# Optimization experiments

Measured on AMD Instinct MI355X. Metric: run time of the kernel, lower is better.

## Reference

```python
import jax, jax.numpy as jnp
import numpy as np

B, S, IN, H = 16, 1024, 1024, 1024

def setup_inputs() -> dict:
    key = jax.random.key(0)
    k1, k2 = jax.random.split(key)
    x = jax.random.normal(k1, (B, S, IN), dtype=jnp.float32)
    # xavier_uniform with gain sqrt(2) over shape [2H, IN]
    limit = np.sqrt(2.0) * np.sqrt(6.0 / (2 * H + IN))
    W = jax.random.uniform(k2, (2 * H, IN), dtype=jnp.float32, minval=-limit, maxval=limit)
    return {"x": x, "W": W}

def reference(x, W):
    # i = x @ W.T -> [B, S, 2H]; split into key/value pre-activations
    i = jnp.einsum('bsi,oi->bso', x, W)
    ik, iv = jnp.split(i, 2, axis=2)          # each [B, S, H]
    mem0 = jnp.zeros((x.shape[0], H, H), dtype=x.dtype)

    def step(mem, kv):
        ik_t, iv_t = kv                        # [B, H] each
        k = jax.nn.relu(ik_t)
        v = jax.nn.relu(iv_t)
        # Hebbian plasticity rule: delta_mem = key outer val
        mem = mem + jnp.einsum('bk,bv->bkv', k, v)
        return mem, (k, v)

    # scan over time: move seq axis to front
    kv_seq = (jnp.swapaxes(ik, 0, 1), jnp.swapaxes(iv, 0, 1))  # [S, B, H]
    mem, (keys, vals) = jax.lax.scan(step, mem0, kv_seq)
    keys = jnp.swapaxes(keys, 0, 1)            # [B, S, H]
    vals = jnp.swapaxes(vals, 0, 1)
    return mem, keys, vals
```

## Files before the change

### kernel.cpp

```cpp
#include <hip/hip_runtime.h>

#define B_  16
#define S_  1024
#define IN_ 1024
#define H_  1024
#define N1  (2*H_)
#define M1  (B_*S_)
#define K1  IN_
#define XN  (M1*IN_)
#define WN  (N1*IN_)
#define LDG 1024

#define BM  256
#define BN  256
#define BK  64
#define CP  257

#define USZ  8192
#define ASZ  16384
#define TBUF 32768

typedef __attribute__((ext_vector_type(8))) short  short8;
typedef __attribute__((ext_vector_type(4))) float  floatx4;

__device__ __forceinline__ unsigned short f2bf(float f) {
    unsigned int u = __float_as_uint(f);
    u += 0x7fffu + ((u >> 16) & 1u);
    return (unsigned short)(u >> 16);
}

#define GLDS16(gp, lp) __builtin_amdgcn_global_load_lds(                      \
    (const __attribute__((address_space(1))) void*)(gp),                      \
    (__attribute__((address_space(3))) void*)(lp), 16, 0, 0)

#define WAITVM(N) { asm volatile("s_waitcnt vmcnt(" #N ")" ::: "memory");     \
                    __builtin_amdgcn_s_barrier();                             \
                    __builtin_amdgcn_sched_barrier(0); }

__global__ __launch_bounds__(256) void convert_kernel(
    const float* __restrict__ x, const float* __restrict__ W,
    unsigned short* __restrict__ xb, unsigned short* __restrict__ Wb)
{
    size_t i = ((size_t)blockIdx.x * 256 + threadIdx.x) * 8;
    const float* src;
    unsigned short* dst;
    if (i < (size_t)XN) { src = x + i; dst = xb + i; }
    else                { src = W + (i - XN); dst = Wb + (i - XN); }
    float4 a = *(const float4*)(src);
    float4 b = *(const float4*)(src + 4);
    ushort4 p = { f2bf(a.x), f2bf(a.y), f2bf(a.z), f2bf(a.w) };
    ushort4 q = { f2bf(b.x), f2bf(b.y), f2bf(b.z), f2bf(b.w) };
    *(ushort4*)(dst)     = p;
    *(ushort4*)(dst + 4) = q;
}

__device__ __forceinline__ void stage_u(
    const unsigned short* Ag, const unsigned short* Bg,
    unsigned short* buf, int op, int kh, int kt, int wave, int lane)
{
    const unsigned short* src = op ? Bg : Ag;
    unsigned short* dst = buf + op * ASZ + kh * USZ;
#pragma unroll
    for (int h = 0; h < 2; ++h) {
        int e   = (wave * 2 + h) * 64 + lane;
        int row = e >> 2, p = e & 3;
        int c   = p ^ (row & 3);
        GLDS16(src + (size_t)row * LDG + kt + kh * 32 + c * 8,
               dst + (wave * 2 + h) * 512);
    }
}

__device__ __forceinline__ void half_tile(
    const unsigned short* bufc, floatx4 (&acc)[8][4], int kc,
    const unsigned short* Ag, const unsigned short* Bg,
    unsigned short* bufn, int ktn, bool st,
    int wave, int lane, int wmw, int wnw, int quad, int r)
{
    const unsigned short* cA = bufc + kc * USZ;
    const unsigned short* cB = bufc + ASZ + kc * USZ;
    const int sw = (quad ^ (r & 3)) * 8;
    short8 bfr[4];
#pragma unroll
    for (int j = 0; j < 4; ++j)
        bfr[j] = *(const short8*)(cB + (wnw + j * 16 + r) * 32 + sw);
#pragma unroll
    for (int mh = 0; mh < 2; ++mh) {
        short8 af[4];
#pragma unroll
        for (int i = 0; i < 4; ++i)
            af[i] = *(const short8*)(cA + (wmw + (mh * 4 + i) * 16 + r) * 32 + sw);
        if (st) stage_u(Ag, Bg, bufn, mh, kc, ktn, wave, lane);
        __builtin_amdgcn_s_setprio(1);
#pragma unroll
        for (int i = 0; i < 4; ++i)
#pragma unroll
            for (int j = 0; j < 4; ++j)
                acc[mh * 4 + i][j] = __builtin_amdgcn_mfma_f32_16x16x32_bf16(
                    af[i], bfr[j], acc[mh * 4 + i][j], 0, 0, 0);
        __builtin_amdgcn_s_setprio(0);
    }
}

__device__ __forceinline__ void gemm_core(
    const unsigned short* Ag, const unsigned short* Bg,
    unsigned short* lds, floatx4 (&acc)[8][4], int wave, int lane)
{
    const int quad = lane >> 4, r = lane & 15;
    const int wmw  = (wave >> 2) * 128;
    const int wnw  = (wave & 3) * 64;

    stage_u(Ag, Bg, lds, 0, 0, 0, wave, lane);
    stage_u(Ag, Bg, lds, 1, 0, 0, wave, lane);
    stage_u(Ag, Bg, lds, 0, 1, 0, wave, lane);
    stage_u(Ag, Bg, lds, 1, 1, 0, wave, lane);

    for (int t = 0; t < 15; ++t) {
        unsigned short* bufc = lds + (t & 1) * TBUF;
        unsigned short* bufn = lds + ((t + 1) & 1) * TBUF;
        const int ktn = (t + 1) * BK;
        WAITVM(4)
        half_tile(bufc, acc, 0, Ag, Bg, bufn, ktn, true, wave, lane, wmw, wnw, quad, r);
        WAITVM(4)
        half_tile(bufc, acc, 1, Ag, Bg, bufn, ktn, true, wave, lane, wmw, wnw, quad, r);
    }
    {
        unsigned short* bufc = lds + TBUF;
        WAITVM(4)
        half_tile(bufc, acc, 0, Ag, Bg, bufc, 0, false, wave, lane, wmw, wnw, quad, r);
        WAITVM(0)
        half_tile(bufc, acc, 1, Ag, Bg, bufc, 0, false, wave, lane, wmw, wnw, quad, r);
    }
    __syncthreads();
}

__global__ __launch_bounds__(512, 2) void gemm1_kernel(
    const unsigned short* __restrict__ xb, const unsigned short* __restrict__ Wb,
    float* __restrict__ out,
    unsigned short* __restrict__ kT, unsigned short* __restrict__ vT)
{
    __shared__ unsigned short lds[65536];

    const int tid  = threadIdx.x;
    const int wave = tid >> 6, lane = tid & 63;
    const int quad = lane >> 4, r = lane & 15;
    const int wmw  = (wave >> 2) * 128;
    const int wnw  = (wave & 3) * 64;

    const int L   = blockIdx.x;
    const int xcd = L & 7, s = L >> 3;
    const int mt  = xcd * 8 + (s >> 3);
    const int nt  = s & 7;
    const int m0  = mt * BM, n0 = nt * BN;

    const unsigned short* Ag = xb + (size_t)m0 * K1;
    const unsigned short* Bg = Wb + (size_t)n0 * K1;

    floatx4 acc[8][4] = {};
    gemm_core(Ag, Bg, lds, acc, wave, lane);

    const bool isKeys = (nt < 4);
    float* outKV    = out + (isKeys ? (size_t)M1 * H_ : (size_t)2 * M1 * H_);
    const int ncol0 = isKeys ? n0 : (n0 - 1024);

#pragma unroll
    for (int f = 0; f < 8; ++f)
#pragma unroll
        for (int j = 0; j < 4; ++j)
#pragma unroll
            for (int d = 0; d < 4; ++d) {
                int row_l = wmw + f * 16 + quad * 4 + d;
                int col_l = wnw + j * 16 + r;
                outKV[(size_t)(m0 + row_l) * H_ + ncol0 + col_l] =
                    fmaxf(acc[f][j][d], 0.0f);
            }

    unsigned short* wsT = isKeys ? kT : vT;
    const int b  = m0 >> 10;
    const int s0 = m0 & 1023;
    unsigned short* dstB = wsT + (size_t)b * H_ * S_ + (size_t)ncol0 * S_ + s0;

#pragma unroll
    for (int ch = 0; ch < 2; ++ch) {
        if ((wave >> 2) == ch) {
#pragma unroll
            for (int f = 0; f < 8; ++f)
#pragma unroll
                for (int j = 0; j < 4; ++j)
#pragma unroll
                    for (int d = 0; d < 4; ++d) {
                        int lrow = f * 16 + quad * 4 + d;
                        int col  = wnw + j * 16 + r;
                        lds[lrow * CP + col] = f2bf(fmaxf(acc[f][j][d], 0.0f));
                    }
        }
        __syncthreads();
#pragma unroll
        for (int it = 0; it < 16; ++it) {
            int o   = it * 512 + tid;
            int n_l = o >> 5;
            int m4  = (o & 31) * 4;
            ushort4 v;
            v.x = lds[(m4 + 0) * CP + n_l];
            v.y = lds[(m4 + 1) * CP + n_l];
            v.z = lds[(m4 + 2) * CP + n_l];
            v.w = lds[(m4 + 3) * CP + n_l];
            *(ushort4*)(dstB + (size_t)n_l * S_ + ch * 128 + m4) = v;
        }
        __syncthreads();
    }
}

__global__ __launch_bounds__(512, 2) void gemm2_kernel(
    const unsigned short* __restrict__ kT, const unsigned short* __restrict__ vT,
    float* __restrict__ mem)
{
    __shared__ unsigned short lds[65536];

    const int tid  = threadIdx.x;
    const int wave = tid >> 6, lane = tid & 63;
    const int quad = lane >> 4, r = lane & 15;
    const int wmw  = (wave >> 2) * 128;
    const int wnw  = (wave & 3) * 64;

    const int L   = blockIdx.x;
    const int xcd = L & 7, s = L >> 3;
    const int b   = xcd * 2 + (s >> 4);
    const int tt  = s & 15;
    const int m0  = (tt >> 2) * BM;
    const int n0  = (tt & 3) * BN;

    const unsigned short* Ag = kT + (size_t)b * H_ * S_ + (size_t)m0 * S_;
    const unsigned short* Bg = vT + (size_t)b * H_ * S_ + (size_t)n0 * S_;

    floatx4 acc[8][4] = {};
    gemm_core(Ag, Bg, lds, acc, wave, lane);

    float* outb = mem + (size_t)b * H_ * H_;
#pragma unroll
    for (int f = 0; f < 8; ++f)
#pragma unroll
        for (int j = 0; j < 4; ++j)
#pragma unroll
            for (int d = 0; d < 4; ++d) {
                int row_l = wmw + f * 16 + quad * 4 + d;
                int col_l = wnw + j * 16 + r;
                outb[(size_t)(m0 + row_l) * H_ + n0 + col_l] = acc[f][j][d];
            }
}

extern "C" void kernel_launch(void* const* d_in, const int* in_sizes, int n_in,
                              void* d_out, int out_size, void* d_ws, size_t ws_size,
                              hipStream_t stream) {
    const float* x = (const float*)d_in[0];
    const float* W = (const float*)d_in[1];
    float* out = (float*)d_out;

    unsigned short* xb = (unsigned short*)d_out;
    unsigned short* Wb = xb + (size_t)XN;

    unsigned short* kT = (unsigned short*)d_ws;
    unsigned short* vT = kT + (size_t)B_ * H_ * S_;

    convert_kernel<<<dim3((XN + WN) / 2048), dim3(256), 0, stream>>>(x, W, xb, Wb);

    gemm1_kernel<<<dim3(512), dim3(512), 0, stream>>>(xb, Wb, out, kT, vT);

    gemm2_kernel<<<dim3(256), dim3(512), 0, stream>>>(kT, vT, out);
}
```

Before: 350.8 us.

## Fuse fp32-to-bf16 conversion of x into the GEMM1 A-tile load pipeline

Result: slower. 383.3 us (+9.3%).

```diff
diff --git a/kernel.cpp b/kernel.cpp
--- a/kernel.cpp
+++ b/kernel.cpp
@@ -7,9 +7,7 @@
 #define N1  (2*H_)
 #define M1  (B_*S_)
 #define K1  IN_
-#define XN  (M1*IN_)
 #define WN  (N1*IN_)
-#define LDG 1024
 
 #define BM  256
 #define BN  256
@@ -37,104 +35,93 @@
                     __builtin_amdgcn_s_barrier();                             \
                     __builtin_amdgcn_sched_barrier(0); }
 
-__global__ __launch_bounds__(256) void convert_kernel(
-    const float* __restrict__ x, const float* __restrict__ W,
-    unsigned short* __restrict__ xb, unsigned short* __restrict__ Wb)
+__global__ __launch_bounds__(256) void convert_w(
+    const float* __restrict__ W, unsigned short* __restrict__ Wb)
 {
     size_t i = ((size_t)blockIdx.x * 256 + threadIdx.x) * 8;
-    const float* src;
-    unsigned short* dst;
-    if (i < (size_t)XN) { src = x + i; dst = xb + i; }
-    else                { src = W + (i - XN); dst = Wb + (i - XN); }
-    float4 a = *(const float4*)(src);
-    float4 b = *(const float4*)(src + 4);
+    float4 a = *(const float4*)(W + i);
+    float4 b = *(const float4*)(W + i + 4);
     ushort4 p = { f2bf(a.x), f2bf(a.y), f2bf(a.z), f2bf(a.w) };
     ushort4 q = { f2bf(b.x), f2bf(b.y), f2bf(b.z), f2bf(b.w) };
-    *(ushort4*)(dst)     = p;
-    *(ushort4*)(dst + 4) = q;
-}
-
-__device__ __forceinline__ void stage_u(
-    const unsigned short* Ag, const unsigned short* Bg,
-    unsigned short* buf, int op, int kh, int kt, int wave, int lane)
-{
-    const unsigned short* src = op ? Bg : Ag;
-    unsigned short* dst = buf + op * ASZ + kh * USZ;
+    *(ushort4*)(Wb + i)     = p;
+    *(ushort4*)(Wb + i + 4) = q;
+}
+
+__device__ __forceinline__ void a_issue(const float* Ag, int koff,
+                                        float4 (&s)[2][2], int wave, int lane)
+{
 #pragma unroll
     for (int h = 0; h < 2; ++h) {
         int e   = (wave * 2 + h) * 64 + lane;
-        int row = e >> 2, p = e & 3;
-        int c   = p ^ (row & 3);
-        GLDS16(src + (size_t)row * LDG + kt + kh * 32 + c * 8,
-               dst + (wave * 2 + h) * 512);
-    }
-}
-
-__device__ __forceinline__ void half_tile(
-    const unsigned short* bufc, floatx4 (&acc)[8][4], int kc,
-    const unsigned short* Ag, const unsigned short* Bg,
-    unsigned short* bufn, int ktn, bool st,
-    int wave, int lane, int wmw, int wnw, int quad, int r)
-{
-    const unsigned short* cA = bufc + kc * USZ;
-    const unsigned short* cB = bufc + ASZ + kc * USZ;
-    const int sw = (quad ^ (r & 3)) * 8;
-    short8 bfr[4];
-#pragma unroll
-    for (int j = 0; j < 4; ++j)
-        bfr[j] = *(const short8*)(cB + (wnw + j * 16 + r) * 32 + sw);
-#pragma unroll
-    for (int mh = 0; mh < 2; ++mh) {
-        short8 af[4];
-#pragma unroll
-        for (int i = 0; i < 4; ++i)
-            af[i] = *(const short8*)(cA + (wmw + (mh * 4 + i) * 16 + r) * 32 + sw);
-        if (st) stage_u(Ag, Bg, bufn, mh, kc, ktn, wave, lane);
-        __builtin_amdgcn_s_setprio(1);
-#pragma unroll
-        for (int i = 0; i < 4; ++i)
-#pragma unroll
-            for (int j = 0; j < 4; ++j)
-                acc[mh * 4 + i][j] = __builtin_amdgcn_mfma_f32_16x16x32_bf16(
-                    af[i], bfr[j], acc[mh * 4 + i][j], 0, 0, 0);
-        __builtin_amdgcn_s_setprio(0);
-    }
-}
-
-__device__ __forceinline__ void gemm_core(
-    const unsigned short* Ag, const unsigned short* Bg,
-    unsigned short* lds, floatx4 (&acc)[8][4], int wave, int lane)
-{
-    const int quad = lane >> 4, r = lane & 15;
-    const int wmw  = (wave >> 2) * 128;
-    const int wnw  = (wave & 3) * 64;
-
-    stage_u(Ag, Bg, lds, 0, 0, 0, wave, lane);
-    stage_u(Ag, Bg, lds, 1, 0, 0, wave, lane);
-    stage_u(Ag, Bg, lds, 0, 1, 0, wave, lane);
-    stage_u(Ag, Bg, lds, 1, 1, 0, wave, lane);
-
-    for (int t = 0; t < 15; ++t) {
-        unsigned short* bufc = lds + (t & 1) * TBUF;
-        unsigned short* bufn = lds + ((t + 1) & 1) * TBUF;
-        const int ktn = (t + 1) * BK;
-        WAITVM(4)
-        half_tile(bufc, acc, 0, Ag, Bg, bufn, ktn, true, wave, lane, wmw, wnw, quad, r);
-        WAITVM(4)
-        half_tile(bufc, acc, 1, Ag, Bg, bufn, ktn, true, wave, lane, wmw, wnw, quad, r);
-    }
-    {
-        unsigned short* bufc = lds + TBUF;
-        WAITVM(4)
-        half_tile(bufc, acc, 0, Ag, Bg, bufc, 0, false, wave, lane, wmw, wnw, quad, r);
-        WAITVM(0)
-        half_tile(bufc, acc, 1, Ag, Bg, bufc, 0, false, wave, lane, wmw, wnw, quad, r);
-    }
-    __syncthreads();
+        int row = e >> 2, pp = e & 3;
+        int c   = pp ^ (row & 3);
+        const float* src = Ag + (size_t)row * 1024 + koff + c * 8;
+        s[h][0] = *(const float4*)(src);
+        s[h][1] = *(const float4*)(src + 4);
+    }
+}
+
+__device__ __forceinline__ void a_write(unsigned short* ubase,
+                                        const float4 (&s)[2][2], int wave, int lane)
+{
+#pragma unroll
+    for (int h = 0; h < 2; ++h) {
+        unsigned int o0, o1, o2, o3;
+        asm("v_cvt_pk_bf16_f32 %0, %1, %2" : "=v"(o0) : "v"(s[h][0].x), "v"(s[h][0].y));
+        asm("v_cvt_pk_bf16_f32 %0, %1, %2" : "=v"(o1) : "v"(s[h][0].z), "v"(s[h][0].w));
+        asm("v_cvt_pk_bf16_f32 %0, %1, %2" : "=v"(o2) : "v"(s[h][1].x), "v"(s[h][1].y));
+        asm("v_cvt_pk_bf16_f32 %0, %1, %2" : "=v"(o3) : "v"(s[h][1].z), "v"(s[h][1].w));
+        uint4 w = { o0, o1, o2, o3 };
+        *(uint4*)(ubase + (wave * 2 + h) * 512 + lane * 8) = w;
+    }
+}
+
+__device__ __forceinline__ void b_stage(const unsigned short* Bg,
+                                        unsigned short* buf, int kh, int koff,
+                                        int wave, int lane)
+{
+#pragma unroll
+    for (int h = 0; h < 2; ++h) {
+        int e   = (wave * 2 + h) * 64 + lane;
+        int row = e >> 2, pp = e & 3;
+        int c   = pp ^ (row & 3);
+        GLDS16(Bg + (size_t)row * 1024 + koff + c * 8,
+               buf + ASZ + kh * USZ + (wave * 2 + h) * 512);
+    }
+}
+
+#define PHASE(bc_, bn_, kh_, SET, W_, I_, BS_, kA_, kB_, VM_)                 \
+{                                                                             \
+    asm volatile("s_waitcnt vmcnt(" VM_ ") lgkmcnt(0)" ::: "memory");         \
+    __builtin_amdgcn_s_barrier();                                             \
+    __builtin_amdgcn_sched_barrier(0);                                        \
+    const unsigned short* cA = (bc_) + (kh_) * USZ;                           \
+    const unsigned short* cB = (bc_) + ASZ + (kh_) * USZ;                     \
+    short8 bfr[4], af0[4], af1[4];                                            \
+    _Pragma("unroll") for (int j = 0; j < 4; ++j)                             \
+        bfr[j] = *(const short8*)(cB + (wnw + j * 16 + r) * 32 + sw);         \
+    _Pragma("unroll") for (int i = 0; i < 4; ++i)                             \
+        af0[i] = *(const short8*)(cA + (wmw + i * 16 + r) * 32 + sw);         \
+    _Pragma("unroll") for (int i = 0; i < 4; ++i)                             \
+        af1[i] = *(const short8*)(cA + (wmw + (4 + i) * 16 + r) * 32 + sw);   \
+    if (W_) a_write((bn_) + (kh_) * USZ, SET, wave, lane);                    \
+    if (I_) a_issue(Ag, (kA_), SET, wave, lane);                              \
+    if (BS_) b_stage(Bg, (bn_), (kh_), (kB_), wave, lane);                    \
+    __builtin_amdgcn_s_setprio(1);                                            \
+    _Pragma("unroll") for (int i = 0; i < 4; ++i)                             \
+        _Pragma("unroll") for (int j = 0; j < 4; ++j)                         \
+            acc[i][j] = __builtin_amdgcn_mfma_f32_16x16x32_bf16(              \
+                af0[i], bfr[j], acc[i][j], 0, 0, 0);                          \
+    _Pragma("unroll") for (int i = 0; i < 4; ++i)                             \
+        _Pragma("unroll") for (int j = 0; j < 4; ++j)                         \
+            acc[4 + i][j] = __builtin_amdgcn_mfma_f32_16x16x32_bf16(          \
+                af1[i], bfr[j], acc[4 + i][j], 0, 0, 0);                      \
+    __builtin_amdgcn_s_setprio(0);                                            \
+    __builtin_amdgcn_sched_barrier(0);                                        \
 }
 
 __global__ __launch_bounds__(512, 2) void gemm1_kernel(
-    const unsigned short* __restrict__ xb, const unsigned short* __restrict__ Wb,
+    const float* __restrict__ x, const unsigned short* __restrict__ Wb,
     float* __restrict__ out,
     unsigned short* __restrict__ kT, unsigned short* __restrict__ vT)
 {
@@ -145,6 +132,7 @@
     const int quad = lane >> 4, r = lane & 15;
     const int wmw  = (wave >> 2) * 128;
     const int wnw  = (wave & 3) * 64;
+    const int sw   = (quad ^ (r & 3)) * 8;
 
     const int L   = blockIdx.x;
     const int xcd = L & 7, s = L >> 3;
@@ -152,11 +140,41 @@
     const int nt  = s & 7;
     const int m0  = mt * BM, n0 = nt * BN;
 
-    const unsigned short* Ag = xb + (size_t)m0 * K1;
+    const float*          Ag = x  + (size_t)m0 * K1;
     const unsigned short* Bg = Wb + (size_t)n0 * K1;
 
     floatx4 acc[8][4] = {};
-    gemm_core(Ag, Bg, lds, acc, wave, lane);
+    float4  s0[2][2], s1[2][2];
+
+    a_issue(Ag, 0 * 32, s0, wave, lane);
+    a_issue(Ag, 1 * 32, s1, wave, lane);
+    asm volatile("s_waitcnt vmcnt(4)" ::: "memory");
+    a_write(lds + 0 * USZ, s0, wave, lane);
+    asm volatile("s_waitcnt vmcnt(0)" ::: "memory");
+    a_write(lds + 1 * USZ, s1, wave, lane);
+    a_issue(Ag, 2 * 32, s0, wave, lane);
+    b_stage(Bg, lds, 0, 0 * 32, wave, lane);
+    a_issue(Ag, 3 * 32, s1, wave, lane);
+    b_stage(Bg, lds, 1, 1 * 32, wave, lane);
+
+    for (int t = 0; t < 14; ++t) {
+        unsigned short* bc = lds + (t & 1) * TBUF;
+        unsigned short* bn = lds + ((t + 1) & 1) * TBUF;
+        PHASE(bc, bn, 0, s0, 1, 1, 1, (2 * t + 4) * 32, (2 * t + 2) * 32, "6")
+        PHASE(bc, bn, 1, s1, 1, 1, 1, (2 * t + 5) * 32, (2 * t + 3) * 32, "6")
+    }
+    {
+        unsigned short* bc = lds;
+        unsigned short* bn = lds + TBUF;
+        PHASE(bc, bn, 0, s0, 1, 0, 1, 0, 30 * 32, "6")
+        PHASE(bc, bn, 1, s1, 1, 0, 1, 0, 31 * 32, "2")
+    }
+    {
+        unsigned short* bc = lds + TBUF;
+        PHASE(bc, bc, 0, s0, 0, 0, 0, 0, 0, "2")
+        PHASE(bc, bc, 1, s1, 0, 0, 0, 0, 0, "0")
+    }
+    __syncthreads();
 
     const bool isKeys = (nt < 4);
     float* outKV    = out + (isKeys ? (size_t)M1 * H_ : (size_t)2 * M1 * H_);
@@ -176,8 +194,8 @@
 
     unsigned short* wsT = isKeys ? kT : vT;
     const int b  = m0 >> 10;
-    const int s0 = m0 & 1023;
-    unsigned short* dstB = wsT + (size_t)b * H_ * S_ + (size_t)ncol0 * S_ + s0;
+    const int sq = m0 & 1023;
+    unsigned short* dstB = wsT + (size_t)b * H_ * S_ + (size_t)ncol0 * S_ + sq;
 
 #pragma unroll
     for (int ch = 0; ch < 2; ++ch) {
@@ -210,6 +228,85 @@
     }
 }
 
+__device__ __forceinline__ void stage_u(
+    const unsigned short* Ag, const unsigned short* Bg,
+    unsigned short* buf, int op, int kh, int kt, int wave, int lane)
+{
+    const unsigned short* src = op ? Bg : Ag;
+    unsigned short* dst = buf + op * ASZ + kh * USZ;
+#pragma unroll
+    for (int h = 0; h < 2; ++h) {
+        int e   = (wave * 2 + h) * 64 + lane;
+        int row = e >> 2, p = e & 3;
+        int c   = p ^ (row & 3);
+        GLDS16(src + (size_t)row * 1024 + kt + kh * 32 + c * 8,
+               dst + (wave * 2 + h) * 512);
+    }
+}
+
+__device__ __forceinline__ void half_tile(
+    const unsigned short* bufc, floatx4 (&acc)[8][4], int kc,
+    const unsigned short* Ag, const unsigned short* Bg,
+    unsigned short* bufn, int ktn, bool st,
+    int wave, int lane, int wmw, int wnw, int quad, int r)
+{
+    const unsigned short* cA = bufc + kc * USZ;
+    const unsigned short* cB = bufc + ASZ + kc * USZ;
+    const int sw = (quad ^ (r & 3)) * 8;
+    short8 bfr[4];
+#pragma unroll
+    for (int j = 0; j < 4; ++j)
+        bfr[j] = *(const short8*)(cB + (wnw + j * 16 + r) * 32 + sw);
+#pragma unroll
+    for (int mh = 0; mh < 2; ++mh) {
+        short8 af[4];
+#pragma unroll
+        for (int i = 0; i < 4; ++i)
+            af[i] = *(const short8*)(cA + (wmw + (mh * 4 + i) * 16 + r) * 32 + sw);
+        if (st) stage_u(Ag, Bg, bufn, mh, kc, ktn, wave, lane);
+        __builtin_amdgcn_s_setprio(1);
+#pragma unroll
+        for (int i = 0; i < 4; ++i)
+#pragma unroll
+            for (int j = 0; j < 4; ++j)
+                acc[mh * 4 + i][j] = __builtin_amdgcn_mfma_f32_16x16x32_bf16(
+                    af[i], bfr[j], acc[mh * 4 + i][j], 0, 0, 0);
+        __builtin_amdgcn_s_setprio(0);
+    }
+}
+
+__device__ __forceinline__ void gemm_core(
+    const unsigned short* Ag, const unsigned short* Bg,
+    unsigned short* lds, floatx4 (&acc)[8][4], int wave, int lane)
+{
+    const int quad = lane >> 4, r = lane & 15;
+    const int wmw  = (wave >> 2) * 128;
+    const int wnw  = (wave & 3) * 64;
+
+    stage_u(Ag, Bg, lds, 0, 0, 0, wave, lane);
+    stage_u(Ag, Bg, lds, 1, 0, 0, wave, lane);
+    stage_u(Ag, Bg, lds, 0, 1, 0, wave, lane);
+    stage_u(Ag, Bg, lds, 1, 1, 0, wave, lane);
+
+    for (int t = 0; t < 15; ++t) {
+        unsigned short* bufc = lds + (t & 1) * TBUF;
+        unsigned short* bufn = lds + ((t + 1) & 1) * TBUF;
+        const int ktn = (t + 1) * BK;
+        WAITVM(4)
+        half_tile(bufc, acc, 0, Ag, Bg, bufn, ktn, true, wave, lane, wmw, wnw, quad, r);
+        WAITVM(4)
+        half_tile(bufc, acc, 1, Ag, Bg, bufn, ktn, true, wave, lane, wmw, wnw, quad, r);
+    }
+    {
+        unsigned short* bufc = lds + TBUF;
+        WAITVM(4)
+        half_tile(bufc, acc, 0, Ag, Bg, bufc, 0, false, wave, lane, wmw, wnw, quad, r);
+        WAITVM(0)
+        half_tile(bufc, acc, 1, Ag, Bg, bufc, 0, false, wave, lane, wmw, wnw, quad, r);
+    }
+    __syncthreads();
+}
+
 __global__ __launch_bounds__(512, 2) void gemm2_kernel(
     const unsigned short* __restrict__ kT, const unsigned short* __restrict__ vT,
     float* __restrict__ mem)
@@ -255,15 +352,14 @@
     const float* W = (const float*)d_in[1];
     float* out = (float*)d_out;
 
-    unsigned short* xb = (unsigned short*)d_out;
-    unsigned short* Wb = xb + (size_t)XN;
+    unsigned short* Wb = (unsigned short*)d_out;
 
     unsigned short* kT = (unsigned short*)d_ws;
     unsigned short* vT = kT + (size_t)B_ * H_ * S_;
 
-    convert_kernel<<<dim3((XN + WN) / 2048), dim3(256), 0, stream>>>(x, W, xb, Wb);
-
-    gemm1_kernel<<<dim3(512), dim3(512), 0, stream>>>(xb, Wb, out, kT, vT);
+    convert_w<<<dim3(WN / 2048), dim3(256), 0, stream>>>(W, Wb);
+
+    gemm1_kernel<<<dim3(512), dim3(512), 0, stream>>>(x, Wb, out, kT, vT);
 
     gemm2_kernel<<<dim3(256), dim3(512), 0, stream>>>(kT, vT, out);
 }
```

## Retile mem GEMM to 128x128 blocks with single-buffered inline k-loop

Applied to the files above, without the earlier changes.

Measured after the change: 352.7 us. Within noise of the previous version (+0.5%).

```diff
diff --git a/kernel.cpp b/kernel.cpp
--- a/kernel.cpp
+++ b/kernel.cpp
@@ -9,7 +9,6 @@
 #define K1  IN_
 #define XN  (M1*IN_)
 #define WN  (N1*IN_)
-#define LDG 1024
 
 #define BM  256
 #define BN  256
@@ -65,7 +64,7 @@
         int e   = (wave * 2 + h) * 64 + lane;
         int row = e >> 2, p = e & 3;
         int c   = p ^ (row & 3);
-        GLDS16(src + (size_t)row * LDG + kt + kh * 32 + c * 8,
+        GLDS16(src + (size_t)row * 1024 + kt + kh * 32 + c * 8,
                dst + (wave * 2 + h) * 512);
     }
 }
@@ -210,41 +209,76 @@
     }
 }
 
-__global__ __launch_bounds__(512, 2) void gemm2_kernel(
+__global__ __launch_bounds__(256, 4) void gemm2_kernel(
     const unsigned short* __restrict__ kT, const unsigned short* __restrict__ vT,
     float* __restrict__ mem)
 {
-    __shared__ unsigned short lds[65536];
+    __shared__ unsigned short lds[16384];
 
     const int tid  = threadIdx.x;
     const int wave = tid >> 6, lane = tid & 63;
     const int quad = lane >> 4, r = lane & 15;
-    const int wmw  = (wave >> 2) * 128;
-    const int wnw  = (wave & 3) * 64;
+    const int wm   = (wave >> 1) * 64;
+    const int wn   = (wave & 1) * 64;
+    const int sw   = (quad ^ (r & 3)) * 8;
 
     const int L   = blockIdx.x;
     const int xcd = L & 7, s = L >> 3;
-    const int b   = xcd * 2 + (s >> 4);
-    const int tt  = s & 15;
-    const int m0  = (tt >> 2) * BM;
-    const int n0  = (tt & 3) * BN;
+    const int b   = xcd * 2 + (s >> 6);
+    const int t   = s & 63;
+    const int m0  = (t >> 3) * 128;
+    const int n0  = (t & 7) * 128;
 
     const unsigned short* Ag = kT + (size_t)b * H_ * S_ + (size_t)m0 * S_;
     const unsigned short* Bg = vT + (size_t)b * H_ * S_ + (size_t)n0 * S_;
 
-    floatx4 acc[8][4] = {};
-    gemm_core(Ag, Bg, lds, acc, wave, lane);
+    floatx4 acc[4][4] = {};
+
+    for (int kt = 0; kt < S_; kt += 64) {
+        __syncthreads();
+#pragma unroll
+        for (int h = 0; h < 4; ++h) {
+            int e   = (wave * 4 + h) * 64 + lane;
+            int kh  = e >> 9, i2 = e & 511;
+            int row = i2 >> 2, p = i2 & 3;
+            int c   = p ^ (row & 3);
+            size_t goff = (size_t)row * 1024 + kt + kh * 32 + c * 8;
+            GLDS16(Ag + goff, lds + (size_t)e * 8);
+            GLDS16(Bg + goff, lds + 8192 + (size_t)e * 8);
+        }
+        __syncthreads();
+#pragma unroll
+        for (int sc = 0; sc < 2; ++sc) {
+            const unsigned short* cA = lds + sc * 4096;
+            const unsigned short* cB = lds + 8192 + sc * 4096;
+            short8 af[4], bfr[4];
+#pragma unroll
+            for (int i = 0; i < 4; ++i)
+                af[i]  = *(const short8*)(cA + (wm + i * 16 + r) * 32 + sw);
+#pragma unroll
+            for (int j = 0; j < 4; ++j)
+                bfr[j] = *(const short8*)(cB + (wn + j * 16 + r) * 32 + sw);
+            __builtin_amdgcn_s_setprio(1);
+#pragma unroll
+            for (int i = 0; i < 4; ++i)
+#pragma unroll
+                for (int j = 0; j < 4; ++j)
+                    acc[i][j] = __builtin_amdgcn_mfma_f32_16x16x32_bf16(
+                        af[i], bfr[j], acc[i][j], 0, 0, 0);
+            __builtin_amdgcn_s_setprio(0);
+        }
+    }
 
     float* outb = mem + (size_t)b * H_ * H_;
 #pragma unroll
-    for (int f = 0; f < 8; ++f)
+    for (int i = 0; i < 4; ++i)
 #pragma unroll
         for (int j = 0; j < 4; ++j)
 #pragma unroll
             for (int d = 0; d < 4; ++d) {
-                int row_l = wmw + f * 16 + quad * 4 + d;
-                int col_l = wnw + j * 16 + r;
-                outb[(size_t)(m0 + row_l) * H_ + n0 + col_l] = acc[f][j][d];
+                int row_l = wm + i * 16 + quad * 4 + d;
+                int col_l = wn + j * 16 + r;
+                outb[(size_t)(m0 + row_l) * H_ + n0 + col_l] = acc[i][j][d];
             }
 }
 
@@ -265,5 +299,5 @@
 
     gemm1_kernel<<<dim3(512), dim3(512), 0, stream>>>(xb, Wb, out, kT, vT);
 
-    gemm2_kernel<<<dim3(256), dim3(512), 0, stream>>>(kT, vT, out);
-}
+    gemm2_kernel<<<dim3(1024), dim3(256), 0, stream>>>(kT, vT, out);
+}
```

## Restructure GEMM mainloop into 4-slot ring with register double-buffered fragments

Applied to the files above, without the earlier changes.

Result: no change. 352.7 us (+0.5%).

```diff
diff --git a/kernel.cpp b/kernel.cpp
--- a/kernel.cpp
+++ b/kernel.cpp
@@ -9,16 +9,11 @@
 #define K1  IN_
 #define XN  (M1*IN_)
 #define WN  (N1*IN_)
-#define LDG 1024
 
 #define BM  256
 #define BN  256
-#define BK  64
 #define CP  257
-
-#define USZ  8192
-#define ASZ  16384
-#define TBUF 32768
+#define SLOT 16384
 
 typedef __attribute__((ext_vector_type(8))) short  short8;
 typedef __attribute__((ext_vector_type(4))) float  floatx4;
@@ -54,51 +49,48 @@
     *(ushort4*)(dst + 4) = q;
 }
 
-__device__ __forceinline__ void stage_u(
+__device__ __forceinline__ void stage_phase(
     const unsigned short* Ag, const unsigned short* Bg,
-    unsigned short* buf, int op, int kh, int kt, int wave, int lane)
-{
-    const unsigned short* src = op ? Bg : Ag;
-    unsigned short* dst = buf + op * ASZ + kh * USZ;
+    unsigned short* lds, int q, int wave, int lane)
+{
+    unsigned short* slot = lds + (q & 3) * SLOT;
+    const int kt = q * 32;
 #pragma unroll
     for (int h = 0; h < 2; ++h) {
         int e   = (wave * 2 + h) * 64 + lane;
         int row = e >> 2, p = e & 3;
         int c   = p ^ (row & 3);
-        GLDS16(src + (size_t)row * LDG + kt + kh * 32 + c * 8,
-               dst + (wave * 2 + h) * 512);
+        size_t go = (size_t)row * 1024 + kt + c * 8;
+        GLDS16(Ag + go, slot + (wave * 2 + h) * 512);
+        GLDS16(Bg + go, slot + 8192 + (wave * 2 + h) * 512);
     }
 }
 
-__device__ __forceinline__ void half_tile(
-    const unsigned short* bufc, floatx4 (&acc)[8][4], int kc,
-    const unsigned short* Ag, const unsigned short* Bg,
-    unsigned short* bufn, int ktn, bool st,
-    int wave, int lane, int wmw, int wnw, int quad, int r)
-{
-    const unsigned short* cA = bufc + kc * USZ;
-    const unsigned short* cB = bufc + ASZ + kc * USZ;
-    const int sw = (quad ^ (r & 3)) * 8;
-    short8 bfr[4];
+__device__ __forceinline__ void read_frags(
+    const unsigned short* lds, int q, short8 (&fa)[8], short8 (&fb)[4],
+    int wmw, int wnw, int r, int sw)
+{
+    const unsigned short* cA = lds + (q & 3) * SLOT;
+    const unsigned short* cB = cA + 8192;
+#pragma unroll
+    for (int i = 0; i < 8; ++i)
+        fa[i] = *(const short8*)(cA + (wmw + i * 16 + r) * 32 + sw);
 #pragma unroll
     for (int j = 0; j < 4; ++j)
-        bfr[j] = *(const short8*)(cB + (wnw + j * 16 + r) * 32 + sw);
-#pragma unroll
-    for (int mh = 0; mh < 2; ++mh) {
-        short8 af[4];
-#pragma unroll
-        for (int i = 0; i < 4; ++i)
-            af[i] = *(const short8*)(cA + (wmw + (mh * 4 + i) * 16 + r) * 32 + sw);
-        if (st) stage_u(Ag, Bg, bufn, mh, kc, ktn, wave, lane);
-        __builtin_amdgcn_s_setprio(1);
-#pragma unroll
-        for (int i = 0; i < 4; ++i)
-#pragma unroll
-            for (int j = 0; j < 4; ++j)
-                acc[mh * 4 + i][j] = __builtin_amdgcn_mfma_f32_16x16x32_bf16(
-                    af[i], bfr[j], acc[mh * 4 + i][j], 0, 0, 0);
-        __builtin_amdgcn_s_setprio(0);
-    }
+        fb[j] = *(const short8*)(cB + (wnw + j * 16 + r) * 32 + sw);
+}
+
+__device__ __forceinline__ void mfma32(
+    floatx4 (&acc)[8][4], const short8 (&fa)[8], const short8 (&fb)[4])
+{
+    __builtin_amdgcn_s_setprio(1);
+#pragma unroll
+    for (int i = 0; i < 8; ++i)
+#pragma unroll
+        for (int j = 0; j < 4; ++j)
+            acc[i][j] = __builtin_amdgcn_mfma_f32_16x16x32_bf16(
+                fa[i], fb[j], acc[i][j], 0, 0, 0);
+    __builtin_amdgcn_s_setprio(0);
 }
 
 __device__ __forceinline__ void gemm_core(
@@ -108,28 +100,33 @@
     const int quad = lane >> 4, r = lane & 15;
     const int wmw  = (wave >> 2) * 128;
     const int wnw  = (wave & 3) * 64;
-
-    stage_u(Ag, Bg, lds, 0, 0, 0, wave, lane);
-    stage_u(Ag, Bg, lds, 1, 0, 0, wave, lane);
-    stage_u(Ag, Bg, lds, 0, 1, 0, wave, lane);
-    stage_u(Ag, Bg, lds, 1, 1, 0, wave, lane);
-
-    for (int t = 0; t < 15; ++t) {
-        unsigned short* bufc = lds + (t & 1) * TBUF;
-        unsigned short* bufn = lds + ((t + 1) & 1) * TBUF;
-        const int ktn = (t + 1) * BK;
+    const int sw   = (quad ^ (r & 3)) * 8;
+
+    short8 F0a[8], F1a[8];
+    short8 F0b[4], F1b[4];
+
+    stage_phase(Ag, Bg, lds, 0, wave, lane);
+    stage_phase(Ag, Bg, lds, 1, wave, lane);
+    stage_phase(Ag, Bg, lds, 2, wave, lane);
+    asm volatile("s_waitcnt vmcnt(8)" ::: "memory");
+    __builtin_amdgcn_s_barrier();
+    __builtin_amdgcn_sched_barrier(0);
+    read_frags(lds, 0, F0a, F0b, wmw, wnw, r, sw);
+
+    for (int p = 0; p < 30; p += 2) {
         WAITVM(4)
-        half_tile(bufc, acc, 0, Ag, Bg, bufn, ktn, true, wave, lane, wmw, wnw, quad, r);
+        read_frags(lds, p + 1, F1a, F1b, wmw, wnw, r, sw);
+        stage_phase(Ag, Bg, lds, p + 3, wave, lane);
+        mfma32(acc, F0a, F0b);
         WAITVM(4)
-        half_tile(bufc, acc, 1, Ag, Bg, bufn, ktn, true, wave, lane, wmw, wnw, quad, r);
+        read_frags(lds, p + 2, F0a, F0b, wmw, wnw, r, sw);
+        if (p + 4 < 32) stage_phase(Ag, Bg, lds, p + 4, wave, lane);
+        mfma32(acc, F1a, F1b);
     }
-    {
-        unsigned short* bufc = lds + TBUF;
-        WAITVM(4)
-        half_tile(bufc, acc, 0, Ag, Bg, bufc, 0, false, wave, lane, wmw, wnw, quad, r);
-        WAITVM(0)
-        half_tile(bufc, acc, 1, Ag, Bg, bufc, 0, false, wave, lane, wmw, wnw, quad, r);
-    }
+    WAITVM(0)
+    read_frags(lds, 31, F1a, F1b, wmw, wnw, r, sw);
+    mfma32(acc, F0a, F0b);
+    mfma32(acc, F1a, F1b);
     __syncthreads();
 }
 
```
